# Optimization experiments

Hardware: AMD Instinct MI355X
Metric: run time of the kernel (lower is better)

The kernel has to match this reference:

```python
import jax, jax.numpy as jnp
import numpy as np

GROUP_SIZE = 128


def setup_inputs() -> dict:
    key = jax.random.key(0)
    k1, k2, k3 = jax.random.split(key, 3)
    x = (jax.random.normal(k1, (4, 2048, 4096), dtype=jnp.float32)).astype(jnp.float16)
    packed_weight = jax.random.randint(k2, (512, 11008), 0, 2147483647, dtype=jnp.int32)
    scales = jax.random.uniform(k3, (32, 11008), dtype=jnp.float32).astype(jnp.float16)
    return {"x": x, "packed_weight": packed_weight, "scales": scales}


def _dequantize(packed_weight, scales):
    # packed_weight: [K//8, N] int32, 8 nibbles per int32 (nibble i at bits 4i..4i+3)
    # scales: [K//GROUP_SIZE, N]
    Kp, N = packed_weight.shape
    K = Kp * 8
    shifts = (jnp.arange(8, dtype=jnp.int32) * 4)[None, :, None]      # [1,8,1]
    nibbles = (packed_weight[:, None, :] >> shifts) & 15              # [K//8,8,N]
    vals = nibbles.reshape(K, N).astype(jnp.float32)                  # [K,N]
    sc = jnp.repeat(scales.astype(jnp.float32), GROUP_SIZE, axis=0)   # [K,N]
    return (vals - 8.0) / 7.5 * sc


def reference(x, packed_weight, scales):
    K = packed_weight.shape[0] * 8
    N = packed_weight.shape[1]
    deq = _dequantize(packed_weight, scales)                 # [K,N] fp32
    x2 = x.reshape(-1, K).astype(jnp.float32)                # [M,K] fp32 accumulate
    out = jnp.matmul(x2, deq).astype(jnp.float16)            # [M,N] fp16 store
    return out.reshape(*x.shape[:-1], N)
```

## Files before the change

kernel.cpp:

```cpp
#include <hip/hip_runtime.h>
#include <stdint.h>

typedef __attribute__((ext_vector_type(8))) _Float16 half8;
typedef __attribute__((ext_vector_type(2))) _Float16 half2v;
typedef __attribute__((ext_vector_type(4))) float floatx4;
typedef __attribute__((ext_vector_type(4))) uint32_t uint4v;

#define KDIM 4096
#define NDIM 11008
#define NKT 64

#define GLOAD_LDS16(gsrc, ldst)                                                        \
  __builtin_amdgcn_global_load_lds(                                                    \
      (const __attribute__((address_space(1))) void*)(gsrc),                           \
      (__attribute__((address_space(3))) void*)(ldst), 16, 0, 0)

static __device__ __forceinline__ uint32_t pkrtz(float a, float b) {
  auto h = __builtin_amdgcn_cvt_pkrtz(a, b);
  return __builtin_bit_cast(uint32_t, h);
}

static __device__ __forceinline__ half8 dq8(uint32_t q, half2v ssv) {
  half2v off; off[0] = (_Float16)(-1032.0f); off[1] = (_Float16)(-1032.0f);
  const uint32_t a0 = (q & 0x000F000Fu) | 0x64006400u;
  const uint32_t a1 = ((q >> 4) & 0x000F000Fu) | 0x64006400u;
  const uint32_t a2 = ((q >> 8) & 0x000F000Fu) | 0x64006400u;
  const uint32_t a3 = ((q >> 12) & 0x000F000Fu) | 0x64006400u;
  const uint32_t p0 = __builtin_amdgcn_perm(a1, a0, 0x05040100u);
  const uint32_t p1 = __builtin_amdgcn_perm(a3, a2, 0x05040100u);
  const uint32_t p2 = __builtin_amdgcn_perm(a1, a0, 0x07060302u);
  const uint32_t p3 = __builtin_amdgcn_perm(a3, a2, 0x07060302u);
  uint4v u;
  u[0] = __builtin_bit_cast(uint32_t, (__builtin_bit_cast(half2v, p0) + off) * ssv);
  u[1] = __builtin_bit_cast(uint32_t, (__builtin_bit_cast(half2v, p1) + off) * ssv);
  u[2] = __builtin_bit_cast(uint32_t, (__builtin_bit_cast(half2v, p2) + off) * ssv);
  u[3] = __builtin_bit_cast(uint32_t, (__builtin_bit_cast(half2v, p3) + off) * ssv);
  return __builtin_bit_cast(half8, u);
}

__global__ __launch_bounds__(256)
void l4b_prep(const float* __restrict__ in, _Float16* __restrict__ out, int n8) {
  int i = blockIdx.x * 256 + threadIdx.x;
  if (i < n8) {
    floatx4 v0 = ((const floatx4*)in)[2 * i];
    floatx4 v1 = ((const floatx4*)in)[2 * i + 1];
    uint4v u;
    u[0] = pkrtz(v0[0], v0[1]); u[1] = pkrtz(v0[2], v0[3]);
    u[2] = pkrtz(v1[0], v1[1]); u[3] = pkrtz(v1[2], v1[3]);
    ((uint4v*)out)[i] = u;
  }
}

__global__ __launch_bounds__(512, 2)
void l4b_main(const _Float16* __restrict__ XH,
              const int* __restrict__ PW,
              const float* __restrict__ SC,
              float* __restrict__ OUT)
{
  __shared__ alignas(16) _Float16 la[2][256 * 64];
  __shared__ alignas(16) _Float16 lb[2][256 * 64];

  const int tid  = threadIdx.x;
  const int lane = tid & 63;
  const int wave = tid >> 6;

  const int cpx = (int)gridDim.x >> 3;
  const int wg  = ((int)blockIdx.x & 7) * cpx + ((int)blockIdx.x >> 3);
  const int by  = wg / 43;
  const int bx  = wg - by * 43;
  const int64_t brow = (int64_t)by * 256;
  const int     bcol = bx * 256;

  const int wr = (wave >> 2) * 128;
  const int wc = (wave & 3) * 64;
  const int fr = lane & 15;
  const int fq = lane >> 4;

  floatx4 acc[8][4];
#pragma unroll
  for (int i = 0; i < 8; ++i)
#pragma unroll
    for (int j = 0; j < 4; ++j) acc[i][j] = (floatx4)(0.0f);

  const int arow8 = lane >> 3;
  const int aslot = (lane & 7) ^ arow8;
  const _Float16* const asrc0 =
      XH + (brow + wave * 32 + arow8) * (int64_t)KDIM + aslot * 8;

  const int bc  = tid & 255;
  const int bkq = tid >> 8;
  const int*   const pwcol = PW + bcol + bc;
  const float* const sccol = SC + bcol + bc;

  int   rw[4];
  float rsc;

#define DMA_A(t, b)                                                        \
  do {                                                                     \
    _Pragma("unroll") for (int g8 = 0; g8 < 4; ++g8)                       \
        GLOAD_LDS16(asrc0 + (int64_t)g8 * 8 * KDIM + (t) * 64,             \
                    &la[b][(wave * 32 + g8 * 8) * 64]);                    \
  } while (0)

#define LOADB(t)                                                           \
  do {                                                                     \
    const int* pp = pwcol + ((t) * 8 + bkq) * NDIM;                        \
    _Pragma("unroll") for (int j_ = 0; j_ < 4; ++j_)                       \
        rw[j_] = pp[j_ * 2 * NDIM];                                        \
    rsc = sccol[(int64_t)((t) >> 1) * NDIM];                               \
  } while (0)

#define WRITE_B(dst)                                                       \
  do {                                                                     \
    const _Float16 ss = (_Float16)(rsc * (1.0f / 7.5f));                   \
    half2v sv; sv[0] = ss; sv[1] = ss;                                     \
    _Pragma("unroll") for (int j_ = 0; j_ < 4; ++j_) {                     \
      half8 v = dq8((uint32_t)rw[j_], sv);                                 \
      const int kp = bkq + 2 * j_;                                         \
      *(half8*)&(dst)[bc * 64 + ((kp ^ (bc & 7)) * 8)] = v;                \
    }                                                                      \
  } while (0)

#define READ_B4(ksl)                                                       \
  _Pragma("unroll") for (int fn_ = 0; fn_ < 4; ++fn_) {                    \
    const int n_ = wc + fn_ * 16 + fr;                                     \
    bfr[fn_] = *(const half8*)&lbp[n_ * 64 + (((ksl) ^ (n_ & 7)) * 8)];    \
  }

#define READ_A4(fm0, ksl)                                                  \
  _Pragma("unroll") for (int fm_ = 0; fm_ < 4; ++fm_) {                    \
    const int m_ = wr + ((fm0) + fm_) * 16 + fr;                           \
    af[fm_] = *(const half8*)&lap[m_ * 64 + (((ksl) ^ (m_ & 7)) * 8)];     \
  }

#define MFMA16(fm0)                                                        \
  __builtin_amdgcn_s_setprio(1);                                           \
  _Pragma("unroll") for (int fm_ = 0; fm_ < 4; ++fm_)                      \
  _Pragma("unroll") for (int fn_ = 0; fn_ < 4; ++fn_)                      \
      acc[(fm0) + fm_][fn_] = __builtin_amdgcn_mfma_f32_16x16x32_f16(      \
          af[fm_], bfr[fn_], acc[(fm0) + fm_][fn_], 0, 0, 0);              \
  __builtin_amdgcn_s_setprio(0);

#define PH_BAR()                                                           \
  do {                                                                     \
    __builtin_amdgcn_sched_barrier(0);                                     \
    __builtin_amdgcn_s_barrier();                                          \
    __builtin_amdgcn_sched_barrier(0);                                     \
  } while (0)

  LOADB(0);
  DMA_A(0, 0);
  WRITE_B(lb[0]);
  __builtin_amdgcn_sched_barrier(0);
  asm volatile("s_waitcnt vmcnt(0) lgkmcnt(0)" ::: "memory");
  __builtin_amdgcn_s_barrier();
  __builtin_amdgcn_sched_barrier(0);

  for (int kt = 0; kt < NKT; ++kt) {
    const int buf = kt & 1;
    const _Float16* lap = la[buf];
    const _Float16* lbp = lb[buf];
    _Float16* const lbn = lb[buf ^ 1];
    const bool havep = (kt + 1 < NKT);

    half8 af[4], bfr[4];

    READ_B4(fq);
    READ_A4(0, fq);
    if (havep) {
      LOADB(kt + 1);
      DMA_A(kt + 1, buf ^ 1);
    }
    PH_BAR();
    MFMA16(0);
    PH_BAR();

    READ_A4(4, fq);
    PH_BAR();
    MFMA16(4);
    PH_BAR();

    READ_B4(4 + fq);
    READ_A4(0, 4 + fq);
    if (havep) WRITE_B(lbn);
    PH_BAR();
    MFMA16(0);
    PH_BAR();

    READ_A4(4, 4 + fq);
    PH_BAR();
    MFMA16(4);
    __builtin_amdgcn_sched_barrier(0);
    asm volatile("s_waitcnt vmcnt(0) lgkmcnt(0)" ::: "memory");
    __builtin_amdgcn_s_barrier();
    __builtin_amdgcn_sched_barrier(0);
  }

#pragma unroll
  for (int fm = 0; fm < 8; ++fm)
#pragma unroll
    for (int fn = 0; fn < 4; ++fn)
#pragma unroll
      for (int r = 0; r < 4; ++r) {
        const int64_t row = brow + wr + fm * 16 + fq * 4 + r;
        const int     col = bcol + wc + fn * 16 + fr;
        OUT[row * NDIM + col] = acc[fm][fn][r];
      }
}

__global__ __launch_bounds__(512, 2)
void l4b_fb(const float* __restrict__ X, const int* __restrict__ PW,
            const float* __restrict__ SC, float* __restrict__ OUT)
{
  __shared__ alignas(16) _Float16 fla[2][256 * 64];
  __shared__ alignas(16) _Float16 flb[2][256 * 64];

  const int tid  = threadIdx.x;
  const int lane = tid & 63;
  const int wave = tid >> 6;

  const int cpx = (int)gridDim.x >> 3;
  const int wg  = ((int)blockIdx.x & 7) * cpx + ((int)blockIdx.x >> 3);
  const int by  = wg / 43;
  const int bx  = wg - by * 43;
  const int64_t brow = (int64_t)by * 256;
  const int     bcol = bx * 256;

  const int wr = (wave >> 2) * 128;
  const int wc = (wave & 3) * 64;
  const int fr = lane & 15;
  const int fq = lane >> 4;

  floatx4 acc[8][4];
#pragma unroll
  for (int i = 0; i < 8; ++i)
#pragma unroll
    for (int j = 0; j < 4; ++j) acc[i][j] = (floatx4)(0.0f);

  const int ar = tid >> 1;
  const int ah = tid & 1;
  const float* const aptr = X + (brow + ar) * (int64_t)KDIM + ah * 32;
  const int bc  = tid & 255;
  const int bkq = tid >> 8;
  const int*   const pwcol = PW + bcol + bc;
  const float* const sccol = SC + bcol + bc;

  floatx4 ra[8];
  int     rwf[4];
  float   rsc;

#define F_LOAD_A(t)                                                        \
  do {                                                                     \
    const float* ap = aptr + (t) * 64;                                     \
    _Pragma("unroll") for (int i_ = 0; i_ < 8; ++i_)                       \
        ra[i_] = *(const floatx4*)(ap + i_ * 4);                           \
  } while (0)

#define F_LOAD_B(t)                                                        \
  do {                                                                     \
    const int* pp = pwcol + ((t) * 8 + bkq) * NDIM;                        \
    _Pragma("unroll") for (int j_ = 0; j_ < 4; ++j_)                       \
        rwf[j_] = pp[j_ * 2 * NDIM];                                       \
    rsc = sccol[(int64_t)((t) >> 1) * NDIM];                               \
  } while (0)

#define F_WRITE_A(dst)                                                     \
  do {                                                                     \
    _Pragma("unroll") for (int i2 = 0; i2 < 4; ++i2) {                     \
      uint4v u;                                                            \
      u[0] = pkrtz(ra[2 * i2][0], ra[2 * i2][1]);                          \
      u[1] = pkrtz(ra[2 * i2][2], ra[2 * i2][3]);                          \
      u[2] = pkrtz(ra[2 * i2 + 1][0], ra[2 * i2 + 1][1]);                  \
      u[3] = pkrtz(ra[2 * i2 + 1][2], ra[2 * i2 + 1][3]);                  \
      const int s_ = ah * 4 + i2;                                          \
      *(half8*)&(dst)[ar * 64 + ((s_ ^ (ar & 7)) * 8)] =                   \
          __builtin_bit_cast(half8, u);                                    \
    }                                                                      \
  } while (0)

#define F_WRITE_B(dst)                                                     \
  do {                                                                     \
    const _Float16 ssf = (_Float16)(rsc * (1.0f / 7.5f));                  \
    half2v sv; sv[0] = ssf; sv[1] = ssf;                                   \
    _Pragma("unroll") for (int j_ = 0; j_ < 4; ++j_) {                     \
      half8 v = dq8((uint32_t)rwf[j_], sv);                                \
      const int kp = bkq + 2 * j_;                                         \
      *(half8*)&(dst)[bc * 64 + ((kp ^ (bc & 7)) * 8)] = v;                \
    }                                                                      \
  } while (0)

#define F_MFMA16(fm0)                                                      \
  __builtin_amdgcn_s_barrier();                                            \
  asm volatile("s_waitcnt lgkmcnt(0)" ::: "memory");                       \
  __builtin_amdgcn_sched_barrier(0);                                       \
  __builtin_amdgcn_s_setprio(1);                                           \
  _Pragma("unroll") for (int fm_ = 0; fm_ < 4; ++fm_)                      \
  _Pragma("unroll") for (int fn_ = 0; fn_ < 4; ++fn_)                      \
      acc[(fm0) + fm_][fn_] = __builtin_amdgcn_mfma_f32_16x16x32_f16(      \
          af[fm_], bfr[fn_], acc[(fm0) + fm_][fn_], 0, 0, 0);              \
  __builtin_amdgcn_s_setprio(0);                                           \
  __builtin_amdgcn_sched_barrier(0);                                       \
  __builtin_amdgcn_s_barrier();                                            \
  __builtin_amdgcn_sched_barrier(0);

  F_LOAD_A(0); F_LOAD_B(0);
  F_WRITE_A(fla[0]); F_WRITE_B(flb[0]);
  F_LOAD_A(1); F_LOAD_B(1);
  asm volatile("s_waitcnt lgkmcnt(0)" ::: "memory");
  __builtin_amdgcn_s_barrier();
  __builtin_amdgcn_sched_barrier(0);

  for (int kt = 0; kt < NKT; ++kt) {
    const int buf = kt & 1;
    const _Float16* lap = fla[buf];
    const _Float16* lbp = flb[buf];
    _Float16* const lan = fla[buf ^ 1];
    _Float16* const lbn = flb[buf ^ 1];
    const bool haveW = (kt + 1 < NKT);
    const bool haveL = (kt + 2 < NKT);

    half8 bfr[4], af[4];

#pragma unroll
    for (int fn_ = 0; fn_ < 4; ++fn_) {
      const int n_ = wc + fn_ * 16 + fr;
      bfr[fn_] = *(const half8*)&lbp[n_ * 64 + ((fq ^ (n_ & 7)) * 8)];
    }
#pragma unroll
    for (int fm_ = 0; fm_ < 4; ++fm_) {
      const int m_ = wr + fm_ * 16 + fr;
      af[fm_] = *(const half8*)&lap[m_ * 64 + ((fq ^ (m_ & 7)) * 8)];
    }
    if (haveW) F_WRITE_A(lan);
    F_MFMA16(0);

#pragma unroll
    for (int fm_ = 0; fm_ < 4; ++fm_) {
      const int m_ = wr + (4 + fm_) * 16 + fr;
      af[fm_] = *(const half8*)&lap[m_ * 64 + ((fq ^ (m_ & 7)) * 8)];
    }
    if (haveL) F_LOAD_A(kt + 2);
    F_MFMA16(4);

#pragma unroll
    for (int fn_ = 0; fn_ < 4; ++fn_) {
      const int n_ = wc + fn_ * 16 + fr;
      bfr[fn_] = *(const half8*)&lbp[n_ * 64 + (((4 + fq) ^ (n_ & 7)) * 8)];
    }
#pragma unroll
    for (int fm_ = 0; fm_ < 4; ++fm_) {
      const int m_ = wr + fm_ * 16 + fr;
      af[fm_] = *(const half8*)&lap[m_ * 64 + (((4 + fq) ^ (m_ & 7)) * 8)];
    }
    if (haveW) F_WRITE_B(lbn);
    F_MFMA16(0);

#pragma unroll
    for (int fm_ = 0; fm_ < 4; ++fm_) {
      const int m_ = wr + (4 + fm_) * 16 + fr;
      af[fm_] = *(const half8*)&lap[m_ * 64 + (((4 + fq) ^ (m_ & 7)) * 8)];
    }
    if (haveL) F_LOAD_B(kt + 2);
    F_MFMA16(4);
  }

#pragma unroll
  for (int fm = 0; fm < 8; ++fm)
#pragma unroll
    for (int fn = 0; fn < 4; ++fn)
#pragma unroll
      for (int r = 0; r < 4; ++r) {
        const int64_t row = brow + wr + fm * 16 + fq * 4 + r;
        const int     col = bcol + wc + fn * 16 + fr;
        OUT[row * NDIM + col] = acc[fm][fn][r];
      }
}

extern "C" void kernel_launch(void* const* d_in, const int* in_sizes, int n_in,
                              void* d_out, int out_size, void* d_ws, size_t ws_size,
                              hipStream_t stream) {
  const float* X   = (const float*)d_in[0];
  const int*   PW  = (const int*)d_in[1];
  const float* SC  = (const float*)d_in[2];
  float*       OUT = (float*)d_out;

  const int    M     = in_sizes[0] / KDIM;
  const size_t needH = (size_t)in_sizes[0] * 2;
  const int    grid  = (M / 256) * (NDIM / 256);

  if (ws_size >= needH && (M % 256) == 0) {
    _Float16* XH = (_Float16*)d_ws;
    const int n8 = in_sizes[0] / 8;
    l4b_prep<<<(n8 + 255) / 256, 256, 0, stream>>>(X, XH, n8);
    l4b_main<<<grid, 512, 0, stream>>>(XH, PW, SC, OUT);
  } else {
    l4b_fb<<<grid, 512, 0, stream>>>(X, PW, SC, OUT);
  }
}
```

Before: 850.3 us.

## Pre-dequantize weights to fp16 in a separate pass and DMA both operands into LDS

Adds a prep kernel that dequantizes the packed int4 weights into a K-major fp16 buffer in workspace, so the main GEMM loads both A and B with global_load_lds straight into LDS. Per-tile register dequantization and LDS writes of B are removed from the main loop, which is restructured into half-K sub-stages with finer vmcnt waits. In exchange there is an extra kernel launch and roughly 90 MB of fp16 weight written and then read back, versus reading packed int4 each time, and the fast path now needs a larger workspace.

```diff
diff --git a/kernel.cpp b/kernel.cpp
--- a/kernel.cpp
+++ b/kernel.cpp
@@ -51,14 +51,45 @@
   }
 }
 
+__global__ __launch_bounds__(256)
+void l4b_prepB(const int* __restrict__ PW, const float* __restrict__ SC,
+               _Float16* __restrict__ BH) {
+  __shared__ alignas(16) _Float16 lt[64 * 64];
+  const int t  = threadIdx.x;
+  const int nb = NDIM / 64;
+  const int kb = blockIdx.x / nb;
+  const int n0 = (blockIdx.x - kb * nb) * 64;
+  const int kp0 = kb * 8;
+#pragma unroll
+  for (int h = 0; h < 2; ++h) {
+    const int idx  = t + h * 256;
+    const int kp_l = idx >> 6;
+    const int n_l  = idx & 63;
+    const int kp   = kp0 + kp_l;
+    const uint32_t q = (uint32_t)PW[kp * NDIM + n0 + n_l];
+    const float    s = SC[(kp >> 4) * NDIM + n0 + n_l];
+    const _Float16 ss = (_Float16)(s * (1.0f / 7.5f));
+    half2v sv; sv[0] = ss; sv[1] = ss;
+    half8 v = dq8(q, sv);
+    *(half8*)&lt[n_l * 64 + ((kp_l ^ (n_l & 7)) * 8)] = v;
+  }
+  __syncthreads();
+  const int n_l = t >> 2;
+  const int c   = t & 3;
+  uint4v o0 = *(uint4v*)&lt[n_l * 64 + (((c * 2) ^ (n_l & 7)) * 8)];
+  uint4v o1 = *(uint4v*)&lt[n_l * 64 + (((c * 2 + 1) ^ (n_l & 7)) * 8)];
+  _Float16* op = BH + (int64_t)(n0 + n_l) * KDIM + kp0 * 8 + c * 16;
+  *(uint4v*)op       = o0;
+  *(uint4v*)(op + 8) = o1;
+}
+
 __global__ __launch_bounds__(512, 2)
-void l4b_main(const _Float16* __restrict__ XH,
-              const int* __restrict__ PW,
-              const float* __restrict__ SC,
-              float* __restrict__ OUT)
+void l4b_g3(const _Float16* __restrict__ XH,
+            const _Float16* __restrict__ BH,
+            float* __restrict__ OUT)
 {
-  __shared__ alignas(16) _Float16 la[2][256 * 64];
-  __shared__ alignas(16) _Float16 lb[2][256 * 64];
+  __shared__ alignas(16) _Float16 la[2][2][256 * 32];
+  __shared__ alignas(16) _Float16 lb[2][2][256 * 32];
 
   const int tid  = threadIdx.x;
   const int lane = tid & 63;
@@ -82,118 +113,109 @@
 #pragma unroll
     for (int j = 0; j < 4; ++j) acc[i][j] = (floatx4)(0.0f);
 
-  const int arow8 = lane >> 3;
-  const int aslot = (lane & 7) ^ arow8;
-  const _Float16* const asrc0 =
-      XH + (brow + wave * 32 + arow8) * (int64_t)KDIM + aslot * 8;
-
-  const int bc  = tid & 255;
-  const int bkq = tid >> 8;
-  const int*   const pwcol = PW + bcol + bc;
-  const float* const sccol = SC + bcol + bc;
-
-  int   rw[4];
-  float rsc;
-
-#define DMA_A(t, b)                                                        \
+  const int s_l = (lane & 3) ^ ((lane >> 2) & 3) ^ ((lane >> 4) & 3);
+  const _Float16* const asrc =
+      XH + (brow + wave * 32 + (lane >> 2)) * (int64_t)KDIM + s_l * 8;
+  const _Float16* const bsrc =
+      BH + (bcol + wave * 32 + (lane >> 2)) * (int64_t)KDIM + s_l * 8;
+
+  const int rslot = fq ^ (fr & 3) ^ ((fr >> 2) & 3);
+
+#define G3_S(t, kh, bf)                                                    \
   do {                                                                     \
-    _Pragma("unroll") for (int g8 = 0; g8 < 4; ++g8)                       \
-        GLOAD_LDS16(asrc0 + (int64_t)g8 * 8 * KDIM + (t) * 64,             \
-                    &la[b][(wave * 32 + g8 * 8) * 64]);                    \
+    GLOAD_LDS16(asrc + (t) * 64 + (kh) * 32,                               \
+                &la[bf][kh][(wave * 32) * 32]);                            \
+    GLOAD_LDS16(asrc + (int64_t)16 * KDIM + (t) * 64 + (kh) * 32,          \
+                &la[bf][kh][(wave * 32 + 16) * 32]);                       \
+    GLOAD_LDS16(bsrc + (t) * 64 + (kh) * 32,                               \
+                &lb[bf][kh][(wave * 32) * 32]);                            \
+    GLOAD_LDS16(bsrc + (int64_t)16 * KDIM + (t) * 64 + (kh) * 32,          \
+                &lb[bf][kh][(wave * 32 + 16) * 32]);                       \
   } while (0)
 
-#define LOADB(t)                                                           \
-  do {                                                                     \
-    const int* pp = pwcol + ((t) * 8 + bkq) * NDIM;                        \
-    _Pragma("unroll") for (int j_ = 0; j_ < 4; ++j_)                       \
-        rw[j_] = pp[j_ * 2 * NDIM];                                        \
-    rsc = sccol[(int64_t)((t) >> 1) * NDIM];                               \
-  } while (0)
-
-#define WRITE_B(dst)                                                       \
-  do {                                                                     \
-    const _Float16 ss = (_Float16)(rsc * (1.0f / 7.5f));                   \
-    half2v sv; sv[0] = ss; sv[1] = ss;                                     \
-    _Pragma("unroll") for (int j_ = 0; j_ < 4; ++j_) {                     \
-      half8 v = dq8((uint32_t)rw[j_], sv);                                 \
-      const int kp = bkq + 2 * j_;                                         \
-      *(half8*)&(dst)[bc * 64 + ((kp ^ (bc & 7)) * 8)] = v;                \
-    }                                                                      \
-  } while (0)
-
-#define READ_B4(ksl)                                                       \
+#define G3_READ_B4(bf, kh)                                                 \
   _Pragma("unroll") for (int fn_ = 0; fn_ < 4; ++fn_) {                    \
     const int n_ = wc + fn_ * 16 + fr;                                     \
-    bfr[fn_] = *(const half8*)&lbp[n_ * 64 + (((ksl) ^ (n_ & 7)) * 8)];    \
-  }
-
-#define READ_A4(fm0, ksl)                                                  \
+    bfr[fn_] = *(const half8*)&lb[bf][kh][n_ * 32 + rslot * 8];            \
+  }
+
+#define G3_READ_A4(bf, kh, g)                                              \
   _Pragma("unroll") for (int fm_ = 0; fm_ < 4; ++fm_) {                    \
-    const int m_ = wr + ((fm0) + fm_) * 16 + fr;                           \
-    af[fm_] = *(const half8*)&lap[m_ * 64 + (((ksl) ^ (m_ & 7)) * 8)];     \
-  }
-
-#define MFMA16(fm0)                                                        \
-  __builtin_amdgcn_s_setprio(1);                                           \
+    const int m_ = wr + ((g)*4 + fm_) * 16 + fr;                           \
+    af[fm_] = *(const half8*)&la[bf][kh][m_ * 32 + rslot * 8];             \
+  }
+
+#define G3_MFMA16(g)                                                       \
   _Pragma("unroll") for (int fm_ = 0; fm_ < 4; ++fm_)                      \
   _Pragma("unroll") for (int fn_ = 0; fn_ < 4; ++fn_)                      \
-      acc[(fm0) + fm_][fn_] = __builtin_amdgcn_mfma_f32_16x16x32_f16(      \
-          af[fm_], bfr[fn_], acc[(fm0) + fm_][fn_], 0, 0, 0);              \
-  __builtin_amdgcn_s_setprio(0);
-
-#define PH_BAR()                                                           \
-  do {                                                                     \
-    __builtin_amdgcn_sched_barrier(0);                                     \
-    __builtin_amdgcn_s_barrier();                                          \
-    __builtin_amdgcn_sched_barrier(0);                                     \
-  } while (0)
-
-  LOADB(0);
-  DMA_A(0, 0);
-  WRITE_B(lb[0]);
-  __builtin_amdgcn_sched_barrier(0);
-  asm volatile("s_waitcnt vmcnt(0) lgkmcnt(0)" ::: "memory");
-  __builtin_amdgcn_s_barrier();
-  __builtin_amdgcn_sched_barrier(0);
-
-  for (int kt = 0; kt < NKT; ++kt) {
-    const int buf = kt & 1;
-    const _Float16* lap = la[buf];
-    const _Float16* lbp = lb[buf];
-    _Float16* const lbn = lb[buf ^ 1];
-    const bool havep = (kt + 1 < NKT);
-
+      acc[(g)*4 + fm_][fn_] = __builtin_amdgcn_mfma_f32_16x16x32_f16(      \
+          af[fm_], bfr[fn_], acc[(g)*4 + fm_][fn_], 0, 0, 0);
+
+#define G3_SB() __builtin_amdgcn_sched_barrier(0)
+#define G3_BAR() __builtin_amdgcn_s_barrier()
+#define G3_LGKM0() asm volatile("s_waitcnt lgkmcnt(0)" ::: "memory")
+
+#define G3_PHASE(g, WAITC)                                                 \
+  G3_SB(); G3_BAR(); G3_LGKM0(); G3_SB();                                  \
+  __builtin_amdgcn_s_setprio(1);                                           \
+  G3_MFMA16(g);                                                            \
+  __builtin_amdgcn_s_setprio(0);                                           \
+  G3_SB(); WAITC; G3_SB(); G3_BAR(); G3_SB()
+
+#define G3_NOW()
+#define G3_VM8() asm volatile("s_waitcnt vmcnt(8)" ::: "memory")
+#define G3_VM4() asm volatile("s_waitcnt vmcnt(4)" ::: "memory")
+#define G3_VM0() asm volatile("s_waitcnt vmcnt(0)" ::: "memory")
+
+  G3_S(0, 0, 0);
+  G3_S(0, 1, 0);
+  G3_SB(); G3_VM4(); G3_SB();
+  G3_BAR();
+  G3_SB();
+
+  for (int kt = 0; kt < NKT - 1; ++kt) {
+    const int bf = kt & 1;
+    const int nb = bf ^ 1;
     half8 af[4], bfr[4];
 
-    READ_B4(fq);
-    READ_A4(0, fq);
-    if (havep) {
-      LOADB(kt + 1);
-      DMA_A(kt + 1, buf ^ 1);
-    }
-    PH_BAR();
-    MFMA16(0);
-    PH_BAR();
-
-    READ_A4(4, fq);
-    PH_BAR();
-    MFMA16(4);
-    PH_BAR();
-
-    READ_B4(4 + fq);
-    READ_A4(0, 4 + fq);
-    if (havep) WRITE_B(lbn);
-    PH_BAR();
-    MFMA16(0);
-    PH_BAR();
-
-    READ_A4(4, 4 + fq);
-    PH_BAR();
-    MFMA16(4);
-    __builtin_amdgcn_sched_barrier(0);
-    asm volatile("s_waitcnt vmcnt(0) lgkmcnt(0)" ::: "memory");
-    __builtin_amdgcn_s_barrier();
-    __builtin_amdgcn_sched_barrier(0);
+    G3_READ_B4(bf, 0);
+    G3_READ_A4(bf, 0, 0);
+    G3_S(kt + 1, 0, nb);
+    G3_PHASE(0, G3_NOW());
+
+    G3_READ_A4(bf, 0, 1);
+    G3_S(kt + 1, 1, nb);
+    G3_PHASE(1, G3_VM8());
+
+    G3_READ_B4(bf, 1);
+    G3_READ_A4(bf, 1, 0);
+    G3_PHASE(0, G3_NOW());
+
+    G3_READ_A4(bf, 1, 1);
+    G3_PHASE(1, G3_VM4());
+  }
+
+  {
+    const int bf = (NKT - 1) & 1;
+    half8 af[4], bfr[4];
+
+    G3_READ_B4(bf, 0);
+    G3_READ_A4(bf, 0, 0);
+    G3_PHASE(0, G3_NOW());
+
+    G3_READ_A4(bf, 0, 1);
+    G3_PHASE(1, G3_VM0());
+
+    G3_READ_B4(bf, 1);
+    G3_READ_A4(bf, 1, 0);
+    G3_PHASE(0, G3_NOW());
+
+    G3_READ_A4(bf, 1, 1);
+    G3_SB(); G3_BAR(); G3_LGKM0(); G3_SB();
+    __builtin_amdgcn_s_setprio(1);
+    G3_MFMA16(1);
+    __builtin_amdgcn_s_setprio(0);
+    G3_SB();
   }
 
 #pragma unroll
@@ -386,13 +408,16 @@
 
   const int    M     = in_sizes[0] / KDIM;
   const size_t needH = (size_t)in_sizes[0] * 2;
+  const size_t needB = (size_t)KDIM * NDIM * 2;
   const int    grid  = (M / 256) * (NDIM / 256);
 
-  if (ws_size >= needH && (M % 256) == 0) {
+  if (ws_size >= needH + needB && (M % 256) == 0) {
     _Float16* XH = (_Float16*)d_ws;
+    _Float16* BH = (_Float16*)((char*)d_ws + needH);
     const int n8 = in_sizes[0] / 8;
     l4b_prep<<<(n8 + 255) / 256, 256, 0, stream>>>(X, XH, n8);
-    l4b_main<<<grid, 512, 0, stream>>>(XH, PW, SC, OUT);
+    l4b_prepB<<<(KDIM / 64) * (NDIM / 64), 256, 0, stream>>>(PW, SC, BH);
+    l4b_g3<<<grid, 512, 0, stream>>>(XH, BH, OUT);
   } else {
     l4b_fb<<<grid, 512, 0, stream>>>(X, PW, SC, OUT);
   }
```

New measurement: 965.4 us. 13.5% more time.
